# Kernel tuning notes

Hardware: AMD Instinct MI355X
Metric: run time of the kernel (lower is better)

The kernel has to match this reference:

```python
import jax, jax.numpy as jnp
import numpy as np

N = 50000
E = 1600000
D_IN = 128
D_OUT = 128
K_EIG = 4
N_AGG = 3
N_SCALE = 3
AVG_D_LOG = float(np.log(33.0))  # avg_d['log'] for avg degree 32
BN_EPS = 1e-5


def setup_inputs() -> dict:
    key = jax.random.key(0)
    ks = jax.random.split(key, 8)
    h = jax.random.normal(ks[0], (N, D_IN), dtype=jnp.float32)
    eig = jax.random.normal(ks[1], (N, K_EIG), dtype=jnp.float32)
    snorm_n = jax.random.uniform(ks[2], (N, 1), dtype=jnp.float32)
    edge_src = jax.random.randint(ks[3], (E,), 0, N, dtype=jnp.int32)
    edge_dst = jax.random.randint(ks[4], (E,), 0, N, dtype=jnp.int32)
    d_cat = N_AGG * N_SCALE * D_IN  # 1152
    W = jax.random.normal(ks[5], (d_cat, D_OUT), dtype=jnp.float32) / np.sqrt(d_cat)
    b = jnp.zeros((D_OUT,), dtype=jnp.float32)
    bn_gamma = jnp.ones((D_OUT,), dtype=jnp.float32)
    bn_beta = jnp.zeros((D_OUT,), dtype=jnp.float32)
    bn_mean = jax.random.normal(ks[6], (D_OUT,), dtype=jnp.float32) * 0.1
    bn_var = jnp.ones((D_OUT,), dtype=jnp.float32)
    return {"h": h, "eig": eig, "snorm_n": snorm_n, "W": W, "b": b,
            "bn_gamma": bn_gamma, "bn_beta": bn_beta, "bn_mean": bn_mean,
            "bn_var": bn_var, "edge_src": edge_src, "edge_dst": edge_dst}


def reference(h, eig, snorm_n, W, b, bn_gamma, bn_beta, bn_mean, bn_var, edge_src, edge_dst):
    h_in = h
    # --- pretrans_edges: message e = src h; vector_field = eig_src - eig_dst ---
    h_e = h[edge_src]                      # [E, d] gathered edge messages
    vf = eig[edge_src] - eig[edge_dst]     # [E, k_eig]
    w = jnp.abs(vf[:, 0:1])                # dir1 weights [E, 1]

    # --- reduce: multi-aggregator segment reduce over destination nodes ---
    deg = jax.ops.segment_sum(jnp.ones((E,), h.dtype), edge_dst, num_segments=N)  # [N]
    deg_safe = jnp.maximum(deg, 1.0)
    sum_h = jax.ops.segment_sum(h_e, edge_dst, num_segments=N)
    mean_h = sum_h / deg_safe[:, None]
    max_h = jax.ops.segment_max(h_e, edge_dst, num_segments=N)
    max_h = jnp.where(deg[:, None] > 0, max_h, 0.0)  # empty mailbox -> 0
    dir_num = jax.ops.segment_sum(h_e * w, edge_dst, num_segments=N)
    dir_den = jax.ops.segment_sum(w, edge_dst, num_segments=N)  # [N, 1]
    dir_av = dir_num / (dir_den + 1e-30)
    agg = jnp.concatenate([mean_h, max_h, dir_av], axis=1)  # [N, 3d]

    # --- scalers: identity, amplification, attenuation ---
    logD = jnp.log(deg + 1.0)[:, None]
    amp = agg * (logD / AVG_D_LOG)
    att = agg * (AVG_D_LOG / jnp.maximum(logD, 1e-6))
    hcat = jnp.concatenate([agg, amp, att], axis=1)  # [N, 9d]

    # --- posttrans MLP (1 layer, no activation) ---
    out = hcat @ W + b
    # graph norm
    out = out * snorm_n
    # batch norm (eval mode, running stats)
    out = (out - bn_mean) * jax.lax.rsqrt(bn_var + BN_EPS) * bn_gamma + bn_beta
    out = jax.nn.relu(out)
    # residual (in_dim == out_dim)
    out = h_in + out
    # dropout p=0.0 / eval -> identity
    return out
```

## Files before the change

kernel.cpp:

```cpp
#include <hip/hip_runtime.h>
#include <hip/hip_bf16.h>

#define DIN 128
#define KEIG 4
#define BSH 7
#define BCAP 5120
#define ITEMS 16
#define AVG_D_LOG 3.4965075614664802f
#define BN_EPS 1e-5f

typedef __attribute__((ext_vector_type(8))) short bf16x8;
typedef __attribute__((ext_vector_type(4))) float f32x4;
typedef __attribute__((ext_vector_type(2))) float f32x2;

#define GLD16(SRC, DST) __builtin_amdgcn_global_load_lds(                     \
    (const __attribute__((address_space(1))) unsigned int*)(const void*)(SRC),\
    (__attribute__((address_space(3))) unsigned int*)(void*)(DST), 16, 0, 0)

static __device__ inline unsigned short f2bf(float f) {
    union { float f; unsigned u; } v; v.f = f;
    unsigned r = v.u + 0x7FFFu + ((v.u >> 16) & 1u);
    return (unsigned short)(r >> 16);
}
static __device__ inline unsigned pack2bf(float lo, float hi) {
    return (unsigned)f2bf(lo) | ((unsigned)f2bf(hi) << 16);
}
static __device__ inline f32x2 up2(unsigned u) {
    f32x2 r;
    r.x = __int_as_float(u << 16);
    r.y = __int_as_float(u & 0xffff0000u);
    return r;
}


__global__ void k_prep(const float* __restrict__ h, unsigned* __restrict__ hb,
                       const float* __restrict__ W, unsigned short* __restrict__ Wt,
                       const float* __restrict__ eig, float* __restrict__ eig0,
                       int* __restrict__ cursor, int* __restrict__ bcur,
                       int nPairs, int wTotal, int N, int nbk)
{
    int i = blockIdx.x * 256 + threadIdx.x;
    if (i < nPairs) {
        float2 v = reinterpret_cast<const float2*>(h)[i];
        hb[i] = pack2bf(v.x, v.y);
    }
    if (i < wTotal) {
        int k = i % 384;
        int rest = i / 384;
        int col = rest & 127;
        int s = rest >> 7;
        const int ks = k >> 5, kg = (k >> 3) & 3, ko = k & 7;
        const int c = s * 8 + kg * 2 + (col >> 6);
        const int lane = col & 63;
        const size_t idx = (size_t)ks * 12288 + c * 512 + lane * 8 + ko;
        Wt[idx] = f2bf(W[(s * 384 + k) * 128 + col]);
    }
    if (i < N) {
        eig0[i] = eig[(size_t)i * KEIG];
        cursor[i] = 0;
    }
    if (i < nbk) bcur[i] = 0;
}


__global__ void k_bucket(const int* __restrict__ src, const int* __restrict__ dst,
                         const float* __restrict__ eig0, int* __restrict__ bcur,
                         uint2* __restrict__ stag, int E, int nbk)
{
    __shared__ int lcnt[512];
    __shared__ int lbase[512];
    const int t = threadIdx.x;
    for (int b = t; b < nbk; b += 256) lcnt[b] = 0;
    __syncthreads();

    const int e0 = blockIdx.x * (256 * ITEMS);
    int   bky[ITEMS];
    int   rnk[ITEMS];
    uint2 rec[ITEMS];
#pragma unroll
    for (int k = 0; k < ITEMS; ++k) {
        const int e = e0 + t + k * 256;
        if (e < E) {
            const int s = src[e], d = dst[e];
            const float w = fabsf(eig0[s] - eig0[d]);
            rec[k] = make_uint2(((unsigned)f2bf(w) << 16) | (unsigned)s, (unsigned)d);
            bky[k] = d >> BSH;
            rnk[k] = atomicAdd(&lcnt[bky[k]], 1);
        } else bky[k] = -1;
    }
    __syncthreads();
    for (int b = t; b < nbk; b += 256) {
        const int c = lcnt[b];
        lbase[b] = c ? atomicAdd(&bcur[b], c) : 0;
    }
    __syncthreads();
#pragma unroll
    for (int k = 0; k < ITEMS; ++k) {
        if (bky[k] >= 0) {
            const int pos = lbase[bky[k]] + rnk[k];
            if (pos < BCAP) stag[(size_t)bky[k] * BCAP + pos] = rec[k];
        }
    }
}


__global__ void k_group(const int* __restrict__ bcur, const uint2* __restrict__ stag,
                        unsigned* __restrict__ final_, int2* __restrict__ offcnt, int N)
{
    __shared__ uint2 sst[BCAP];
    __shared__ int hcnt[128];
    __shared__ int sbuf[2][128];
    const int b = blockIdx.x;
    const int t = threadIdx.x;
    const int cb = min(bcur[b], BCAP);

    for (int i = t; i < cb; i += 256) sst[i] = stag[(size_t)b * BCAP + i];
    if (t < 128) hcnt[t] = 0;
    __syncthreads();

    int dl[(BCAP + 255) / 256];
    int rk[(BCAP + 255) / 256];
    int nit = 0;
    for (int i = t; i < cb; i += 256) {
        const int d_loc = sst[i].y & 127;
        dl[nit] = d_loc;
        rk[nit] = atomicAdd(&hcnt[d_loc], 1);
        ++nit;
    }
    __syncthreads();

    int cur = 0;
    if (t < 128) sbuf[0][t] = hcnt[t];
    __syncthreads();
    for (int d = 1; d < 128; d <<= 1) {
        if (t < 128) {
            int x = sbuf[cur][t];
            if (t >= d) x += sbuf[cur][t - d];
            sbuf[cur ^ 1][t] = x;
        }
        cur ^= 1;
        __syncthreads();
    }
    const int exb = cur ^ 1;
    if (t < 128) sbuf[exb][t] = sbuf[cur][t] - hcnt[t];
    __syncthreads();

    if (t < 128) {
        const int dg = (b << BSH) + t;
        if (dg < N) offcnt[dg] = make_int2(b * BCAP + sbuf[exb][t], hcnt[t]);
    }
    nit = 0;
    for (int i = t; i < cb; i += 256) {
        final_[(size_t)b * BCAP + sbuf[exb][dl[nit]] + rk[nit]] = sst[i].x;
        ++nit;
    }
}


__global__ void k_hist(const int* __restrict__ dst, int* __restrict__ counts, int E) {
    int e = blockIdx.x * 256 + threadIdx.x;
    if (e < E) atomicAdd(&counts[dst[e]], 1);
}

__global__ void k_part(const int* __restrict__ counts, int* __restrict__ part, int N) {
    __shared__ int red[4];
    const int t = threadIdx.x;
    const int i = blockIdx.x * 256 + t;
    int v = (i < N) ? counts[i] : 0;
    for (int d = 32; d >= 1; d >>= 1) v += __shfl_down(v, d, 64);
    if ((t & 63) == 0) red[t >> 6] = v;
    __syncthreads();
    if (t == 0) part[blockIdx.x] = red[0] + red[1] + red[2] + red[3];
}

__global__ void k_scan1(const int* __restrict__ part, int* __restrict__ partoff,
                        int* __restrict__ total_out, int NB) {
    __shared__ int buf[2][256];
    const int t = threadIdx.x;
    int v = (t < NB) ? part[t] : 0;
    buf[0][t] = v;
    __syncthreads();
    int cur = 0;
    for (int d = 1; d < 256; d <<= 1) {
        int x = buf[cur][t];
        if (t >= d) x += buf[cur][t - d];
        buf[cur ^ 1][t] = x;
        cur ^= 1;
        __syncthreads();
    }
    if (t < NB) partoff[t] = buf[cur][t] - v;
    if (t == 255) *total_out = buf[cur][255];
}

__global__ void k_off(const int* __restrict__ counts, const int* __restrict__ partoff,
                      int* __restrict__ offsets, int* __restrict__ cursor, int N) {
    __shared__ int buf[2][256];
    const int t = threadIdx.x;
    const int i = blockIdx.x * 256 + t;
    int v = (i < N) ? counts[i] : 0;
    buf[0][t] = v;
    __syncthreads();
    int cur = 0;
    for (int d = 1; d < 256; d <<= 1) {
        int x = buf[cur][t];
        if (t >= d) x += buf[cur][t - d];
        buf[cur ^ 1][t] = x;
        cur ^= 1;
        __syncthreads();
    }
    if (i < N) {
        int excl = partoff[blockIdx.x] + buf[cur][t] - v;
        offsets[i] = excl;
        cursor[i]  = excl;
    }
}

__global__ void k_fill_csr(const int* __restrict__ src, const int* __restrict__ dst,
                           const float* __restrict__ eig0, int* __restrict__ cursor,
                           int2* __restrict__ sedge, int E)
{
    int e = blockIdx.x * 256 + threadIdx.x;
    if (e < E) {
        int s = src[e], d = dst[e];
        float w = fabsf(eig0[s] - eig0[d]);
        int pos = atomicAdd(&cursor[d], 1);
        sedge[pos] = make_int2(s, __float_as_int(w));
    }
}


template<bool PACKED>
__launch_bounds__(256, 4)
__global__ void k_agg(const unsigned* __restrict__ hb,
                      const int2* __restrict__ offcnt, const int* __restrict__ offsets,
                      const unsigned* __restrict__ upk, const int2* __restrict__ sedge,
                      unsigned short* __restrict__ agg, float2* __restrict__ scal, int N)
{
    const int tid = threadIdx.x;
    const int qid = tid >> 4;
    const int l16 = tid & 15;
    const int n = blockIdx.x * 16 + qid;
    if (n >= N) return;

    int e0, cnt;
    if (PACKED) { const int2 oc = offcnt[n]; e0 = oc.x; cnt = oc.y; }
    else        { e0 = offsets[n]; cnt = offsets[n + 1] - e0; }

    const uint4* __restrict__ hb4 = reinterpret_cast<const uint4*>(hb);

    f32x2 s2[4], m2[4], d2[4];
    float wsum = 0.f;
#pragma unroll
    for (int f = 0; f < 4; ++f) {
        s2[f] = (f32x2){0.f, 0.f};
        m2[f] = (f32x2){-INFINITY, -INFINITY};
        d2[f] = (f32x2){0.f, 0.f};
    }
    const int clampi = (cnt > 0) ? cnt - 1 : 0;

    uint4 bufA[8], bufB[8];
    float wvA[8], wvB[8];

#define STAGE(BUF, WV, BASE) do {                                        \
    _Pragma("unroll")                                                    \
    for (int j = 0; j < 8; ++j) {                                        \
        int ci = (BASE) + j; ci = ci < clampi ? ci : clampi;             \
        unsigned sidx;                                                   \
        if (PACKED) {                                                    \
            const unsigned u = upk[e0 + ci];                             \
            WV[j] = __int_as_float(u & 0xffff0000u);                     \
            sidx = (u & 0xffffu) << 4;                                   \
        } else {                                                         \
            const int2 v = sedge[e0 + ci];                               \
            WV[j] = __int_as_float(v.y);                                 \
            sidx = ((unsigned)v.x) << 4;                                 \
        }                                                                \
        BUF[j] = hb4[sidx | (unsigned)l16];                              \
    }                                                                    \
} while (0)

#define ACCUM(BUF, WV, BASE) do {                                        \
    _Pragma("unroll")                                                    \
    for (int j = 0; j < 8; ++j) {                                        \
        if ((BASE) + j < cnt) {                                          \
            const float wj = WV[j];                                      \
            const f32x2 wj2 = (f32x2){wj, wj};                           \
            const f32x2 p0 = up2(BUF[j].x), p1 = up2(BUF[j].y);          \
            const f32x2 p2 = up2(BUF[j].z), p3 = up2(BUF[j].w);          \
            s2[0] += p0; s2[1] += p1; s2[2] += p2; s2[3] += p3;          \
            m2[0].x = fmaxf(m2[0].x, p0.x); m2[0].y = fmaxf(m2[0].y, p0.y); \
            m2[1].x = fmaxf(m2[1].x, p1.x); m2[1].y = fmaxf(m2[1].y, p1.y); \
            m2[2].x = fmaxf(m2[2].x, p2.x); m2[2].y = fmaxf(m2[2].y, p2.y); \
            m2[3].x = fmaxf(m2[3].x, p3.x); m2[3].y = fmaxf(m2[3].y, p3.y); \
            d2[0] += p0 * wj2; d2[1] += p1 * wj2;                        \
            d2[2] += p2 * wj2; d2[3] += p3 * wj2;                        \
            wsum += wj;                                                  \
        }                                                                \
    }                                                                    \
} while (0)

    if (cnt > 0) {
        STAGE(bufA, wvA, 0);
        for (int base = 0; base < cnt; base += 16) {
            const bool haveB = (base + 8) < cnt;
            if (haveB) STAGE(bufB, wvB, base + 8);
            ACCUM(bufA, wvA, base);
            if (base + 16 < cnt) STAGE(bufA, wvA, base + 16);
            if (haveB) ACCUM(bufB, wvB, base + 8);
        }
    }
#undef STAGE
#undef ACCUM

    const float degf = (float)cnt;
    const float inv  = 1.0f / fmaxf(degf, 1.0f);
    const float dinv = 1.0f / (wsum + 1e-30f);
    const bool nz = (cnt > 0);
    uint4 pm, px, pd;
    pm.x = pack2bf(s2[0].x * inv, s2[0].y * inv);
    pm.y = pack2bf(s2[1].x * inv, s2[1].y * inv);
    pm.z = pack2bf(s2[2].x * inv, s2[2].y * inv);
    pm.w = pack2bf(s2[3].x * inv, s2[3].y * inv);
    px.x = pack2bf(nz ? m2[0].x : 0.f, nz ? m2[0].y : 0.f);
    px.y = pack2bf(nz ? m2[1].x : 0.f, nz ? m2[1].y : 0.f);
    px.z = pack2bf(nz ? m2[2].x : 0.f, nz ? m2[2].y : 0.f);
    px.w = pack2bf(nz ? m2[3].x : 0.f, nz ? m2[3].y : 0.f);
    pd.x = pack2bf(d2[0].x * dinv, d2[0].y * dinv);
    pd.y = pack2bf(d2[1].x * dinv, d2[1].y * dinv);
    pd.z = pack2bf(d2[2].x * dinv, d2[2].y * dinv);
    pd.w = pack2bf(d2[3].x * dinv, d2[3].y * dinv);

    uint4* aggv = reinterpret_cast<uint4*>(agg);
    const int mt = n >> 6, row = n & 63;
    const size_t b4 = (size_t)mt * 3072 + (size_t)(l16 & 3) * 64 + row;
    const int kshi = l16 >> 2;
    aggv[b4 + (size_t)(0 * 4 + kshi) * 256] = pm;
    aggv[b4 + (size_t)(1 * 4 + kshi) * 256] = px;
    aggv[b4 + (size_t)(2 * 4 + kshi) * 256] = pd;
    if (l16 == 0) {
        const float logD = logf(degf + 1.0f);
        scal[n] = make_float2(logD / AVG_D_LOG, AVG_D_LOG / fmaxf(logD, 1e-6f));
    }
}


__launch_bounds__(256)
__global__ void k_mm(const unsigned short* __restrict__ agg, const float2* __restrict__ scal,
                     const float* __restrict__ h, const float* __restrict__ snorm,
                     const float* __restrict__ bvec, const float* __restrict__ gam,
                     const float* __restrict__ bet, const float* __restrict__ bmean,
                     const float* __restrict__ bvar, const unsigned short* __restrict__ Wt,
                     float* __restrict__ out, int N)
{
    __shared__ char smem[8192 + 49152];
    unsigned short* As = (unsigned short*)smem;
    unsigned short* Bs = (unsigned short*)(smem + 8192);
    float* outS = (float*)(smem + 8192);

    const int tid  = threadIdx.x;
    const int wave = tid >> 6;
    const int lane = tid & 63;
    const int r16  = lane & 15;
    const int kgrp = lane >> 4;
    const int node0 = blockIdx.x * 64;
    const int cb = wave * 32;

    const char* aggbase = (const char*)agg + (size_t)blockIdx.x * 49152;
    const char* wtbase  = (const char*)Wt;

    auto stage = [&](int ks, int bf) {
        {
            char* dst = (char*)As + (size_t)(bf * 4 + wave) * 1024;
            const char* src = aggbase + (size_t)ks * 4096 + wave * 1024 + lane * 16;
            GLD16(src, dst);
        }
#pragma unroll
        for (int i = 0; i < 6; ++i) {
            const int c = wave * 6 + i;
            char* dst = (char*)Bs + (size_t)bf * 24576 + (size_t)c * 1024;
            const char* src = wtbase + (size_t)ks * 24576 + (size_t)c * 1024 + lane * 16;
            GLD16(src, dst);
        }
    };

    f32x4 acc[4][2][3];
#pragma unroll
    for (int m = 0; m < 4; ++m)
#pragma unroll
        for (int ct = 0; ct < 2; ++ct)
#pragma unroll
            for (int sv = 0; sv < 3; ++sv)
                acc[m][ct][sv] = (f32x4){0.f, 0.f, 0.f, 0.f};

    stage(0, 0);
    for (int ks = 0; ks < 12; ++ks) {
        const int bf = ks & 1;
        __syncthreads();
        if (ks + 1 < 12) stage(ks + 1, bf ^ 1);

        bf16x8 a[4], b[6];
#pragma unroll
        for (int m = 0; m < 4; ++m)
            a[m] = *reinterpret_cast<const bf16x8*>(
                &As[((size_t)(bf * 4 + kgrp) * 64 + m * 16 + r16) * 8]);
#pragma unroll
        for (int sv = 0; sv < 3; ++sv)
#pragma unroll
            for (int ct = 0; ct < 2; ++ct)
                b[sv * 2 + ct] = *reinterpret_cast<const bf16x8*>(
                    &Bs[(((size_t)(bf * 3 + sv) * 4 + kgrp) * 128 + cb + ct * 16 + r16) * 8]);
#pragma unroll
        for (int sv = 0; sv < 3; ++sv)
#pragma unroll
            for (int ct = 0; ct < 2; ++ct)
#pragma unroll
                for (int m = 0; m < 4; ++m)
                    acc[m][ct][sv] = __builtin_amdgcn_mfma_f32_16x16x32_bf16(
                        a[m], b[sv * 2 + ct], acc[m][ct][sv], 0, 0, 0);
    }

    __syncthreads();
#pragma unroll
    for (int ct = 0; ct < 2; ++ct) {
        const int col = cb + ct * 16 + r16;
        const float bc  = bvec[col];
        const float mc  = bmean[col];
        const float rs  = rsqrtf(bvar[col] + BN_EPS);
        const float gc  = gam[col];
        const float bec = bet[col];
#pragma unroll
        for (int m = 0; m < 4; ++m) {
#pragma unroll
            for (int r = 0; r < 4; ++r) {
                const int row = m * 16 + kgrp * 4 + r;
                const int n  = node0 + row;
                float sn = 0.f; float2 sc = make_float2(0.f, 0.f);
                if (n < N) { sn = snorm[n]; sc = scal[n]; }
                float v = acc[m][ct][0][r] + sc.x * acc[m][ct][1][r]
                                           + sc.y * acc[m][ct][2][r];
                float y = (v + bc) * sn;
                y = (y - mc) * rs * gc + bec;
                y = fmaxf(y, 0.f);
                outS[row * 132 + col] = y;
            }
        }
    }
    __syncthreads();

    const int rows = (N - node0 < 64) ? (N - node0) : 64;
#pragma unroll
    for (int it = 0; it < 8; ++it) {
        const int idx = it * 256 + tid;
        const int row = idx >> 5;
        const int c4  = idx & 31;
        if (row < rows) {
            const float4 hv = *reinterpret_cast<const float4*>(
                &h[(size_t)(node0 + row) * 128 + c4 * 4]);
            float4 yv = *reinterpret_cast<const float4*>(&outS[row * 132 + c4 * 4]);
            yv.x += hv.x; yv.y += hv.y; yv.z += hv.z; yv.w += hv.w;
            *reinterpret_cast<float4*>(&out[(size_t)(node0 + row) * 128 + c4 * 4]) = yv;
        }
    }
}


extern "C" void kernel_launch(void* const* d_in, const int* in_sizes, int n_in,
                              void* d_out, int out_size, void* d_ws, size_t ws_size,
                              hipStream_t stream)
{
    const float* h     = (const float*)d_in[0];
    const float* eig   = (const float*)d_in[1];
    const float* snorm = (const float*)d_in[2];
    const float* W     = (const float*)d_in[3];
    const float* bvec  = (const float*)d_in[4];
    const float* gam   = (const float*)d_in[5];
    const float* bet   = (const float*)d_in[6];
    const float* bmean = (const float*)d_in[7];
    const float* bvar  = (const float*)d_in[8];
    const int*   esrc  = (const int*)d_in[9];
    const int*   edst  = (const int*)d_in[10];
    float* out = (float*)d_out;

    const int N = in_sizes[0] / DIN;
    const int E = in_sizes[9];
    const int NB = (N + 255) / 256;
    const int nPairs = N * DIN / 2;
    const int wTotal = 3 * 128 * 384;
    const int nbk = (N + 127) >> BSH;
    const int N64 = (N + 63) / 64;
    (void)ws_size; (void)n_in; (void)out_size;

    char* base = (char*)d_ws;
    size_t o = 0;
    auto take = [&](size_t bytes) {
        char* p = base + o;
        o = (o + bytes + 255) & ~(size_t)255;
        return p;
    };
    unsigned* hb       = (unsigned*)take((size_t)nPairs * 4);
    unsigned short* Wt = (unsigned short*)take((size_t)wTotal * 2);
    float* eig0        = (float*)take((size_t)N * 4);
    int* cursor        = (int*)take((size_t)(N + 1) * 4);
    float2* scal       = (float2*)take((size_t)N * 8);

    const size_t agg_bytes  = (size_t)N64 * 49152;
    const size_t stag_bytes = (size_t)nbk * BCAP * 8;
    const size_t shared_bytes = agg_bytes > stag_bytes ? agg_bytes : stag_bytes;

    const size_t bucket_bytes = (size_t)nbk * BCAP * 4
                              + (size_t)N * 8
                              + (size_t)nbk * 4
                              + shared_bytes + 8192;
    const bool bucketOK = (N <= 65536) && (nbk <= 512) && ((o + bucket_bytes) <= ws_size);

    const int gridPrep = (nPairs + 255) / 256;
    const int gridE    = (E + 255) / 256;
    const int gridB    = (E + 256 * ITEMS - 1) / (256 * ITEMS);
    const int gridN16  = (N + 15) / 16;

    if (bucketOK) {
        unsigned* fin   = (unsigned*)take((size_t)nbk * BCAP * 4);
        int2* offcnt    = (int2*)take((size_t)N * 8);
        int* bcur       = (int*)take((size_t)nbk * 4);
        char* shared    = take(shared_bytes);
        uint2* stag     = (uint2*)shared;
        unsigned short* agg = (unsigned short*)shared;

        k_prep<<<gridPrep, 256, 0, stream>>>(h, hb, W, Wt, eig, eig0, cursor, bcur,
                                             nPairs, wTotal, N, nbk);
        k_bucket<<<gridB, 256, 0, stream>>>(esrc, edst, eig0, bcur, stag, E, nbk);
        k_group<<<nbk, 256, 0, stream>>>(bcur, stag, fin, offcnt, N);
        k_agg<true><<<gridN16, 256, 0, stream>>>(hb, offcnt, nullptr, fin, nullptr,
                                                 agg, scal, N);
        k_mm<<<N64, 256, 0, stream>>>(agg, scal, h, snorm, bvec, gam, bet, bmean, bvar,
                                      Wt, out, N);
    } else {
        int* counts  = (int*)take((size_t)(N + 1) * 4);
        int* offsets = (int*)take((size_t)(N + 1) * 4);
        int2* sedge  = (int2*)take((size_t)(E + 16) * 8);
        int* part    = (int*)take((size_t)NB * 4);
        int* partoff = (int*)take((size_t)NB * 4);
        int* bcur    = (int*)take(4096);
        unsigned short* agg = (unsigned short*)take(agg_bytes);

        k_prep<<<gridPrep, 256, 0, stream>>>(h, hb, W, Wt, eig, eig0, counts, bcur,
                                             nPairs, wTotal, N, 1);
        k_hist<<<gridE, 256, 0, stream>>>(edst, counts, E);
        k_part<<<NB, 256, 0, stream>>>(counts, part, N);
        k_scan1<<<1, 256, 0, stream>>>(part, partoff, &offsets[N], NB);
        k_off<<<NB, 256, 0, stream>>>(counts, partoff, offsets, cursor, N);
        k_fill_csr<<<gridE, 256, 0, stream>>>(esrc, edst, eig0, cursor, sedge, E);
        k_agg<false><<<gridN16, 256, 0, stream>>>(hb, nullptr, offsets, nullptr, sedge,
                                                  agg, scal, N);
        k_mm<<<N64, 256, 0, stream>>>(agg, scal, h, snorm, bvec, gam, bet, bmean, bvar,
                                      Wt, out, N);
    }
}
```

Baseline: 159.5 us.

## Single-buffer GEMM LDS for occupancy and add branch-free full-chunk accumulation

The GEMM kernel drops LDS double buffering. Each k-step now loads into a single buffer and synchronises before and after the load, which cuts shared memory from about 57KB to 33KB so more blocks can be resident per CU. The price is that global loads no longer overlap the MFMA work within a block. The aggregation kernel also gains a specialised path for full 8-edge chunks that avoids per-edge bounds checks and pairs edges for max/add.

```diff
diff --git a/kernel.cpp b/kernel.cpp
--- a/kernel.cpp
+++ b/kernel.cpp
@@ -279,7 +279,34 @@
     }                                                                    \
 } while (0)
 
-#define ACCUM(BUF, WV, BASE) do {                                        \
+#define ACCUM_FULL(BUF, WV) do {                                         \
+    _Pragma("unroll")                                                    \
+    for (int jp = 0; jp < 4; ++jp) {                                     \
+        const float wa = WV[2 * jp], wb = WV[2 * jp + 1];                \
+        const f32x2 wa2 = (f32x2){wa, wa}, wb2 = (f32x2){wb, wb};        \
+        const f32x2 a0 = up2(BUF[2 * jp].x),     a1 = up2(BUF[2 * jp].y); \
+        const f32x2 a2 = up2(BUF[2 * jp].z),     a3 = up2(BUF[2 * jp].w); \
+        const f32x2 b0 = up2(BUF[2 * jp + 1].x), b1 = up2(BUF[2 * jp + 1].y); \
+        const f32x2 b2 = up2(BUF[2 * jp + 1].z), b3 = up2(BUF[2 * jp + 1].w); \
+        s2[0] += a0 + b0; s2[1] += a1 + b1;                              \
+        s2[2] += a2 + b2; s2[3] += a3 + b3;                              \
+        m2[0].x = fmaxf(fmaxf(m2[0].x, a0.x), b0.x);                     \
+        m2[0].y = fmaxf(fmaxf(m2[0].y, a0.y), b0.y);                     \
+        m2[1].x = fmaxf(fmaxf(m2[1].x, a1.x), b1.x);                     \
+        m2[1].y = fmaxf(fmaxf(m2[1].y, a1.y), b1.y);                     \
+        m2[2].x = fmaxf(fmaxf(m2[2].x, a2.x), b2.x);                     \
+        m2[2].y = fmaxf(fmaxf(m2[2].y, a2.y), b2.y);                     \
+        m2[3].x = fmaxf(fmaxf(m2[3].x, a3.x), b3.x);                     \
+        m2[3].y = fmaxf(fmaxf(m2[3].y, a3.y), b3.y);                     \
+        d2[0] += a0 * wa2; d2[0] += b0 * wb2;                            \
+        d2[1] += a1 * wa2; d2[1] += b1 * wb2;                            \
+        d2[2] += a2 * wa2; d2[2] += b2 * wb2;                            \
+        d2[3] += a3 * wa2; d2[3] += b3 * wb2;                            \
+        wsum += wa + wb;                                                 \
+    }                                                                    \
+} while (0)
+
+#define ACCUM_TAIL(BUF, WV, BASE) do {                                   \
     _Pragma("unroll")                                                    \
     for (int j = 0; j < 8; ++j) {                                        \
         if ((BASE) + j < cnt) {                                          \
@@ -304,13 +331,18 @@
         for (int base = 0; base < cnt; base += 16) {
             const bool haveB = (base + 8) < cnt;
             if (haveB) STAGE(bufB, wvB, base + 8);
-            ACCUM(bufA, wvA, base);
+            if (base + 8 <= cnt) ACCUM_FULL(bufA, wvA);
+            else                 ACCUM_TAIL(bufA, wvA, base);
             if (base + 16 < cnt) STAGE(bufA, wvA, base + 16);
-            if (haveB) ACCUM(bufB, wvB, base + 8);
+            if (haveB) {
+                if (base + 16 <= cnt) ACCUM_FULL(bufB, wvB);
+                else                  ACCUM_TAIL(bufB, wvB, base + 8);
+            }
         }
     }
 #undef STAGE
-#undef ACCUM
+#undef ACCUM_FULL
+#undef ACCUM_TAIL
 
     const float degf = (float)cnt;
     const float inv  = 1.0f / fmaxf(degf, 1.0f);
@@ -352,10 +384,10 @@
                      const float* __restrict__ bvar, const unsigned short* __restrict__ Wt,
                      float* __restrict__ out, int N)
 {
-    __shared__ char smem[8192 + 49152];
+    __shared__ char smem[33792];
     unsigned short* As = (unsigned short*)smem;
-    unsigned short* Bs = (unsigned short*)(smem + 8192);
-    float* outS = (float*)(smem + 8192);
+    unsigned short* Bs = (unsigned short*)(smem + 4096);
+    float* outS = (float*)smem;
 
     const int tid  = threadIdx.x;
     const int wave = tid >> 6;
@@ -368,16 +400,16 @@
     const char* aggbase = (const char*)agg + (size_t)blockIdx.x * 49152;
     const char* wtbase  = (const char*)Wt;
 
-    auto stage = [&](int ks, int bf) {
+    auto stage = [&](int ks) {
         {
-            char* dst = (char*)As + (size_t)(bf * 4 + wave) * 1024;
+            char* dst = (char*)As + (size_t)wave * 1024;
             const char* src = aggbase + (size_t)ks * 4096 + wave * 1024 + lane * 16;
             GLD16(src, dst);
         }
 #pragma unroll
         for (int i = 0; i < 6; ++i) {
             const int c = wave * 6 + i;
-            char* dst = (char*)Bs + (size_t)bf * 24576 + (size_t)c * 1024;
+            char* dst = (char*)Bs + (size_t)c * 1024;
             const char* src = wtbase + (size_t)ks * 24576 + (size_t)c * 1024 + lane * 16;
             GLD16(src, dst);
         }
@@ -392,23 +424,22 @@
             for (int sv = 0; sv < 3; ++sv)
                 acc[m][ct][sv] = (f32x4){0.f, 0.f, 0.f, 0.f};
 
-    stage(0, 0);
     for (int ks = 0; ks < 12; ++ks) {
-        const int bf = ks & 1;
+        if (ks) __syncthreads();
+        stage(ks);
         __syncthreads();
-        if (ks + 1 < 12) stage(ks + 1, bf ^ 1);
 
         bf16x8 a[4], b[6];
 #pragma unroll
         for (int m = 0; m < 4; ++m)
             a[m] = *reinterpret_cast<const bf16x8*>(
-                &As[((size_t)(bf * 4 + kgrp) * 64 + m * 16 + r16) * 8]);
+                &As[((size_t)kgrp * 64 + m * 16 + r16) * 8]);
 #pragma unroll
         for (int sv = 0; sv < 3; ++sv)
 #pragma unroll
             for (int ct = 0; ct < 2; ++ct)
                 b[sv * 2 + ct] = *reinterpret_cast<const bf16x8*>(
-                    &Bs[(((size_t)(bf * 3 + sv) * 4 + kgrp) * 128 + cb + ct * 16 + r16) * 8]);
+                    &Bs[(((size_t)sv * 4 + kgrp) * 128 + cb + ct * 16 + r16) * 8]);
 #pragma unroll
         for (int sv = 0; sv < 3; ++sv)
 #pragma unroll
```

Measured after the change: 277.6 us. 74.1% more time.

## Process two 64-row tiles per block in k_mm to reuse W tiles

Applied to the files above, without the earlier changes.

Each k_mm block now computes two 64-node tiles against the same staged W slice, halving the number of blocks and the total W traffic from global memory into LDS. Double buffering is removed to shrink shared memory to about 33KB and allow two blocks per CU (launch_bounds 256,2). Accumulators double to 96 f32x4 registers per thread, which raises register pressure, and the loss of prefetch overlap means each k-step now stalls on its own loads.

```diff
diff --git a/kernel.cpp b/kernel.cpp
--- a/kernel.cpp
+++ b/kernel.cpp
@@ -344,122 +344,134 @@
 }
 
 
-__launch_bounds__(256)
+__launch_bounds__(256, 2)
 __global__ void k_mm(const unsigned short* __restrict__ agg, const float2* __restrict__ scal,
                      const float* __restrict__ h, const float* __restrict__ snorm,
                      const float* __restrict__ bvec, const float* __restrict__ gam,
                      const float* __restrict__ bet, const float* __restrict__ bmean,
                      const float* __restrict__ bvar, const unsigned short* __restrict__ Wt,
-                     float* __restrict__ out, int N)
-{
-    __shared__ char smem[8192 + 49152];
+                     float* __restrict__ out, int N, int nT)
+{
+    __shared__ char smem[33792];
     unsigned short* As = (unsigned short*)smem;
     unsigned short* Bs = (unsigned short*)(smem + 8192);
-    float* outS = (float*)(smem + 8192);
+    float* outS = (float*)smem;
 
     const int tid  = threadIdx.x;
     const int wave = tid >> 6;
     const int lane = tid & 63;
     const int r16  = lane & 15;
     const int kgrp = lane >> 4;
-    const int node0 = blockIdx.x * 64;
     const int cb = wave * 32;
 
-    const char* aggbase = (const char*)agg + (size_t)blockIdx.x * 49152;
-    const char* wtbase  = (const char*)Wt;
-
-    auto stage = [&](int ks, int bf) {
-        {
-            char* dst = (char*)As + (size_t)(bf * 4 + wave) * 1024;
-            const char* src = aggbase + (size_t)ks * 4096 + wave * 1024 + lane * 16;
-            GLD16(src, dst);
-        }
+    const int mt0 = blockIdx.x * 2;
+    const int mt1 = (mt0 + 1 < nT) ? (mt0 + 1) : mt0;
+    const char* aggb0 = (const char*)agg + (size_t)mt0 * 49152;
+    const char* aggb1 = (const char*)agg + (size_t)mt1 * 49152;
+    const char* wtbase = (const char*)Wt;
+
+    auto stage = [&](int ks) {
+        GLD16(aggb0 + (size_t)ks * 4096 + wave * 1024 + lane * 16,
+              (char*)As + (size_t)wave * 1024);
+        GLD16(aggb1 + (size_t)ks * 4096 + wave * 1024 + lane * 16,
+              (char*)As + (size_t)(4 + wave) * 1024);
 #pragma unroll
         for (int i = 0; i < 6; ++i) {
             const int c = wave * 6 + i;
-            char* dst = (char*)Bs + (size_t)bf * 24576 + (size_t)c * 1024;
-            const char* src = wtbase + (size_t)ks * 24576 + (size_t)c * 1024 + lane * 16;
-            GLD16(src, dst);
+            GLD16(wtbase + (size_t)ks * 24576 + (size_t)c * 1024 + lane * 16,
+                  (char*)Bs + (size_t)c * 1024);
         }
     };
 
-    f32x4 acc[4][2][3];
-#pragma unroll
-    for (int m = 0; m < 4; ++m)
-#pragma unroll
-        for (int ct = 0; ct < 2; ++ct)
-#pragma unroll
-            for (int sv = 0; sv < 3; ++sv)
-                acc[m][ct][sv] = (f32x4){0.f, 0.f, 0.f, 0.f};
-
-    stage(0, 0);
+    f32x4 acc[2][4][2][3];
+#pragma unroll
+    for (int t = 0; t < 2; ++t)
+#pragma unroll
+        for (int m = 0; m < 4; ++m)
+#pragma unroll
+            for (int ct = 0; ct < 2; ++ct)
+#pragma unroll
+                for (int sv = 0; sv < 3; ++sv)
+                    acc[t][m][ct][sv] = (f32x4){0.f, 0.f, 0.f, 0.f};
+
     for (int ks = 0; ks < 12; ++ks) {
-        const int bf = ks & 1;
+        if (ks) __syncthreads();
+        stage(ks);
         __syncthreads();
-        if (ks + 1 < 12) stage(ks + 1, bf ^ 1);
-
-        bf16x8 a[4], b[6];
-#pragma unroll
-        for (int m = 0; m < 4; ++m)
-            a[m] = *reinterpret_cast<const bf16x8*>(
-                &As[((size_t)(bf * 4 + kgrp) * 64 + m * 16 + r16) * 8]);
+
+        bf16x8 a0[4], a1[4], b[6];
+#pragma unroll
+        for (int m = 0; m < 4; ++m) {
+            a0[m] = *reinterpret_cast<const bf16x8*>(
+                &As[((size_t)kgrp * 64 + m * 16 + r16) * 8]);
+            a1[m] = *reinterpret_cast<const bf16x8*>(
+                &As[((size_t)(4 + kgrp) * 64 + m * 16 + r16) * 8]);
+        }
 #pragma unroll
         for (int sv = 0; sv < 3; ++sv)
 #pragma unroll
             for (int ct = 0; ct < 2; ++ct)
                 b[sv * 2 + ct] = *reinterpret_cast<const bf16x8*>(
-                    &Bs[(((size_t)(bf * 3 + sv) * 4 + kgrp) * 128 + cb + ct * 16 + r16) * 8]);
+                    &Bs[(((size_t)sv * 4 + kgrp) * 128 + cb + ct * 16 + r16) * 8]);
 #pragma unroll
         for (int sv = 0; sv < 3; ++sv)
 #pragma unroll
             for (int ct = 0; ct < 2; ++ct)
 #pragma unroll
-                for (int m = 0; m < 4; ++m)
-                    acc[m][ct][sv] = __builtin_amdgcn_mfma_f32_16x16x32_bf16(
-                        a[m], b[sv * 2 + ct], acc[m][ct][sv], 0, 0, 0);
-    }
-
-    __syncthreads();
-#pragma unroll
-    for (int ct = 0; ct < 2; ++ct) {
-        const int col = cb + ct * 16 + r16;
-        const float bc  = bvec[col];
-        const float mc  = bmean[col];
-        const float rs  = rsqrtf(bvar[col] + BN_EPS);
-        const float gc  = gam[col];
-        const float bec = bet[col];
-#pragma unroll
-        for (int m = 0; m < 4; ++m) {
-#pragma unroll
-            for (int r = 0; r < 4; ++r) {
-                const int row = m * 16 + kgrp * 4 + r;
-                const int n  = node0 + row;
-                float sn = 0.f; float2 sc = make_float2(0.f, 0.f);
-                if (n < N) { sn = snorm[n]; sc = scal[n]; }
-                float v = acc[m][ct][0][r] + sc.x * acc[m][ct][1][r]
-                                           + sc.y * acc[m][ct][2][r];
-                float y = (v + bc) * sn;
-                y = (y - mc) * rs * gc + bec;
-                y = fmaxf(y, 0.f);
-                outS[row * 132 + col] = y;
+                for (int m = 0; m < 4; ++m) {
+                    acc[0][m][ct][sv] = __builtin_amdgcn_mfma_f32_16x16x32_bf16(
+                        a0[m], b[sv * 2 + ct], acc[0][m][ct][sv], 0, 0, 0);
+                    acc[1][m][ct][sv] = __builtin_amdgcn_mfma_f32_16x16x32_bf16(
+                        a1[m], b[sv * 2 + ct], acc[1][m][ct][sv], 0, 0, 0);
+                }
+    }
+
+    __syncthreads();
+#pragma unroll
+    for (int t = 0; t < 2; ++t) {
+        if (t == 1 && mt1 == mt0) break;
+        const int nb = (t ? mt1 : mt0) * 64;
+#pragma unroll
+        for (int ct = 0; ct < 2; ++ct) {
+            const int col = cb + ct * 16 + r16;
+            const float bc  = bvec[col];
+            const float mc  = bmean[col];
+            const float rs  = rsqrtf(bvar[col] + BN_EPS);
+            const float gc  = gam[col];
+            const float bec = bet[col];
+#pragma unroll
+            for (int m = 0; m < 4; ++m) {
+#pragma unroll
+                for (int r = 0; r < 4; ++r) {
+                    const int row = m * 16 + kgrp * 4 + r;
+                    const int n  = nb + row;
+                    float sn = 0.f; float2 sc = make_float2(0.f, 0.f);
+                    if (n < N) { sn = snorm[n]; sc = scal[n]; }
+                    float v = acc[t][m][ct][0][r] + sc.x * acc[t][m][ct][1][r]
+                                                  + sc.y * acc[t][m][ct][2][r];
+                    float y = (v + bc) * sn;
+                    y = (y - mc) * rs * gc + bec;
+                    y = fmaxf(y, 0.f);
+                    outS[row * 132 + col] = y;
+                }
             }
         }
-    }
-    __syncthreads();
-
-    const int rows = (N - node0 < 64) ? (N - node0) : 64;
-#pragma unroll
-    for (int it = 0; it < 8; ++it) {
-        const int idx = it * 256 + tid;
-        const int row = idx >> 5;
-        const int c4  = idx & 31;
-        if (row < rows) {
-            const float4 hv = *reinterpret_cast<const float4*>(
-                &h[(size_t)(node0 + row) * 128 + c4 * 4]);
-            float4 yv = *reinterpret_cast<const float4*>(&outS[row * 132 + c4 * 4]);
-            yv.x += hv.x; yv.y += hv.y; yv.z += hv.z; yv.w += hv.w;
-            *reinterpret_cast<float4*>(&out[(size_t)(node0 + row) * 128 + c4 * 4]) = yv;
-        }
+        __syncthreads();
+        const int rows = (N - nb < 64) ? (N - nb) : 64;
+#pragma unroll
+        for (int it = 0; it < 8; ++it) {
+            const int idx = it * 256 + tid;
+            const int row = idx >> 5;
+            const int c4  = idx & 31;
+            if (row < rows) {
+                const float4 hv = *reinterpret_cast<const float4*>(
+                    &h[(size_t)(nb + row) * 128 + c4 * 4]);
+                float4 yv = *reinterpret_cast<const float4*>(&outS[row * 132 + c4 * 4]);
+                yv.x += hv.x; yv.y += hv.y; yv.z += hv.z; yv.w += hv.w;
+                *reinterpret_cast<float4*>(&out[(size_t)(nb + row) * 128 + c4 * 4]) = yv;
+            }
+        }
+        __syncthreads();
     }
 }
 
@@ -488,6 +500,7 @@
     const int wTotal = 3 * 128 * 384;
     const int nbk = (N + 127) >> BSH;
     const int N64 = (N + 63) / 64;
+    const int N128 = (N + 127) / 128;
     (void)ws_size; (void)n_in; (void)out_size;
 
     char* base = (char*)d_ws;
@@ -532,8 +545,8 @@
         k_group<<<nbk, 256, 0, stream>>>(bcur, stag, fin, offcnt, N);
         k_agg<true><<<gridN16, 256, 0, stream>>>(hb, offcnt, nullptr, fin, nullptr,
                                                  agg, scal, N);
-        k_mm<<<N64, 256, 0, stream>>>(agg, scal, h, snorm, bvec, gam, bet, bmean, bvar,
-                                      Wt, out, N);
+        k_mm<<<N128, 256, 0, stream>>>(agg, scal, h, snorm, bvec, gam, bet, bmean, bvar,
+                                       Wt, out, N, N64);
     } else {
         int* counts  = (int*)take((size_t)(N + 1) * 4);
         int* offsets = (int*)take((size_t)(N + 1) * 4);
@@ -552,7 +565,7 @@
         k_fill_csr<<<gridE, 256, 0, stream>>>(esrc, edst, eig0, cursor, sedge, E);
         k_agg<false><<<gridN16, 256, 0, stream>>>(hb, nullptr, offsets, nullptr, sedge,
                                                   agg, scal, N);
-        k_mm<<<N64, 256, 0, stream>>>(agg, scal, h, snorm, bvec, gam, bet, bmean, bvar,
-                                      Wt, out, N);
-    }
-}
+        k_mm<<<N128, 256, 0, stream>>>(agg, scal, h, snorm, bvec, gam, bet, bmean, bvar,
+                                       Wt, out, N, N64);
+    }
+}
```

After: 150.6 us (median of 2 runs). 1.06x faster.
